# Kernel optimization log

Measured on AMD Instinct MI355X. Metric: run time of the kernel, lower is better.

The kernel has to match this reference:

```python
import jax, jax.numpy as jnp
import numpy as np

MARGIN = 5.0
VAR_FLOOR = 1e-4
BIG = 1e6


def setup_inputs() -> dict:
    key = jax.random.key(0)
    ks = jax.random.split(key, 8)
    B, D, R = 512, 768, 128
    C_new, C_old = 10, 100
    return {
        "features": jax.random.normal(ks[0], (B, D), jnp.float32),
        "labels": jax.random.randint(ks[1], (B,), 0, C_new),
        "new_class_ids": jnp.arange(C_new),
        "cur_means": jax.random.normal(ks[2], (C_new, D), jnp.float32),
        "cur_bases": jax.random.normal(ks[3], (C_new, D, R), jnp.float32),
        "cur_variances": jax.random.uniform(ks[4], (C_new, R + 1), jnp.float32),
        "calibrated_old_means": jax.random.normal(ks[5], (C_old, D), jnp.float32),
        "calibrated_old_bases": jax.random.normal(ks[6], (C_old, D, R), jnp.float32),
        "calibrated_old_variances": jax.random.uniform(ks[7], (C_old, R + 1), jnp.float32),
    }


def _geometry_distance_matrix(z, means, bases, variances):
    # z: [B,D], means: [C,D], bases: [C,D,R], variances: [C,R+1] -> [B,C]
    diff = z[:, None, :] - means[None, :, :]                    # [B,C,D]
    coeff = jnp.einsum('bcd,cdr->bcr', diff, bases)             # [B,C,R]
    eig = jnp.maximum(variances[:, :-1], VAR_FLOOR)             # [C,R]
    res = jnp.maximum(variances[:, -1], VAR_FLOOR)              # [C]
    parallel = jnp.sum(coeff * coeff / eig[None, :, :], axis=-1)  # [B,C]
    recon = jnp.einsum('bcr,cdr->bcd', coeff, bases)            # [B,C,D]
    residual_term = jnp.sum((diff - recon) ** 2, axis=-1) / res[None, :]
    dist = (parallel + residual_term) / z.shape[1]              # normalize_by_dim
    return jnp.nan_to_num(dist, nan=BIG, posinf=BIG, neginf=BIG)


def reference(features, labels, new_class_ids, cur_means, cur_bases, cur_variances,
              calibrated_old_means, calibrated_old_bases, calibrated_old_variances):
    z = jnp.nan_to_num(features, nan=0.0, posinf=0.0, neginf=0.0)  # [B,D]
    labels = labels.reshape(-1)

    own_all = _geometry_distance_matrix(z, cur_means, cur_bases, cur_variances)  # [B,C_new_total]
    old_all = _geometry_distance_matrix(z, calibrated_old_means, calibrated_old_bases,
                                        calibrated_old_variances)               # [B,C_old]
    old_min = jnp.min(old_all, axis=1)                                           # [B]

    # Per-new-class masks; union of class masks reproduces new_mask implicitly.
    masks = (labels[None, :] == new_class_ids[:, None]).astype(z.dtype)          # [K,B]
    counts = masks.sum(axis=1)                                                   # [K]
    denom = jnp.maximum(counts, 1.0)

    own_k = own_all[:, new_class_ids].T                                          # [K,B]
    hinge = jax.nn.relu(MARGIN + own_k - old_min[None, :])                       # [K,B]

    total_k = (hinge * masks).sum(axis=1) / denom
    own_k_mean = (own_k * masks).sum(axis=1) / denom
    old_k_mean = (old_min[None, :] * masks).sum(axis=1) / denom

    valid = (counts > 0).astype(z.dtype)
    n_valid = jnp.maximum(valid.sum(), 1.0)
    total = (total_k * valid).sum() / n_valid
    own = (own_k_mean * valid).sum() / n_valid
    old = (old_k_mean * valid).sum() / n_valid
    return jnp.stack([total, own, old])  # [total, own, old]
```

## Files before the change

### kernel.cpp

```cpp
#include <hip/hip_runtime.h>
#include <hip/hip_bf16.h>
#include <math.h>
#include <stdint.h>

#define B_N   512
#define D_N   768
#define R_N   128
#define C_NEW 10
#define C_OLD 100
#define C_TOT 110
#define MARGIN_F    5.0f
#define VAR_FLOOR_F 1e-4f
#define BIG_F       1e6f

typedef __bf16 bf16;
typedef __bf16 bf16x4 __attribute__((ext_vector_type(4)));
typedef __bf16 bf16x8 __attribute__((ext_vector_type(8)));
typedef float  f32x4  __attribute__((ext_vector_type(4)));

__device__ __forceinline__ float cleanf(float v) { return isfinite(v) ? v : 0.0f; }

__global__ __launch_bounds__(256)
void prep_z(const float* __restrict__ z, bf16* __restrict__ zbf, float* __restrict__ znorm)
{
    const int wave = threadIdx.x >> 6, lane = threadIdx.x & 63;
    const int b = blockIdx.x * 4 + wave;
    const float4* src = (const float4*)(z + (size_t)b * D_N);
    bf16x4* dst = (bf16x4*)(zbf + (size_t)b * D_N);
    float nrm = 0.f;
    #pragma unroll
    for (int i = 0; i < 3; ++i) {
        float4 v = src[lane + i * 64];
        v.x = cleanf(v.x); v.y = cleanf(v.y); v.z = cleanf(v.z); v.w = cleanf(v.w);
        nrm += v.x * v.x + v.y * v.y + v.z * v.z + v.w * v.w;
        bf16x4 w;
        w[0] = (bf16)v.x; w[1] = (bf16)v.y; w[2] = (bf16)v.z; w[3] = (bf16)v.w;
        dst[lane + i * 64] = w;
    }
    #pragma unroll
    for (int off = 32; off >= 1; off >>= 1) nrm += __shfl_xor(nrm, off, 64);
    if (lane == 0) znorm[b] = nrm;
}

__global__ __launch_bounds__(256)
void prep_munorm(const float* __restrict__ cur_means, const float* __restrict__ old_means,
                 float* __restrict__ munorm)
{
    const int c = blockIdx.x;
    const float* mu = (c < C_NEW) ? cur_means + (size_t)c * D_N
                                  : old_means + (size_t)(c - C_NEW) * D_N;
    float p = 0.f;
    for (int d = threadIdx.x; d < D_N; d += 256) p += mu[d] * mu[d];
    #pragma unroll
    for (int off = 32; off >= 1; off >>= 1) p += __shfl_xor(p, off, 64);
    __shared__ float s[4];
    const int wave = threadIdx.x >> 6, lane = threadIdx.x & 63;
    if (lane == 0) s[wave] = p;
    __syncthreads();
    if (threadIdx.x == 0) munorm[c] = s[0] + s[1] + s[2] + s[3];
}

__global__ __launch_bounds__(256)
void transpose_mc(const float* __restrict__ cur_bases, const float* __restrict__ old_bases,
                  const float* __restrict__ cur_means, const float* __restrict__ old_means,
                  bf16* __restrict__ basesT, float* __restrict__ m_c)
{
    const int dt = blockIdx.x, c = blockIdx.y;
    const float* Bc = (c < C_NEW) ? cur_bases + (size_t)c * D_N * R_N
                                  : old_bases + (size_t)(c - C_NEW) * D_N * R_N;
    const float* mu = (c < C_NEW) ? cur_means + (size_t)c * D_N
                                  : old_means + (size_t)(c - C_NEW) * D_N;
    __shared__ bf16 T[128][132];
    __shared__ float sMu[128];
    const int t = threadIdx.x;
    const int d0 = dt * 128;
    if (t < 128) sMu[t] = mu[d0 + t];

    #pragma unroll 4
    for (int it = 0; it < 16; ++it) {
        int q = it * 256 + t;
        int d = q >> 5, rr = (q & 31) * 4;
        float4 v = *(const float4*)(Bc + (size_t)(d0 + d) * R_N + rr);
        T[rr + 0][d] = (bf16)v.x;
        T[rr + 1][d] = (bf16)v.y;
        T[rr + 2][d] = (bf16)v.z;
        T[rr + 3][d] = (bf16)v.w;
    }
    __syncthreads();

    #pragma unroll 4
    for (int it = 0; it < 16; ++it) {
        int q = it * 256 + t;
        int r = q >> 5, dd = (q & 31) * 4;
        ushort4 w = *(const ushort4*)&T[r][dd];
        *(ushort4*)(basesT + (size_t)c * R_N * D_N + (size_t)r * D_N + d0 + dd) = w;
    }

    {
        int r = t & 127, dh = t >> 7;
        float p = 0.f;
        #pragma unroll 8
        for (int k = 0; k < 64; ++k) {
            int d = dh * 64 + k;
            p += sMu[d] * (float)T[r][d];
        }
        atomicAdd(&m_c[c * R_N + r], p);
    }
}

__global__ __launch_bounds__(256)
void gram(const bf16* __restrict__ basesT, bf16* __restrict__ G)
{
    const int c = blockIdx.x;
    const bf16* Tc = basesT + (size_t)c * R_N * D_N;
    __shared__ bf16 sT[128][72];
    const int tid = threadIdx.x, wave = tid >> 6, lane = tid & 63;
    const int quad = lane >> 4, l15 = lane & 15;
    const int wr = (wave >> 1) * 64, wc = (wave & 1) * 64;

    f32x4 acc[4][4];
    #pragma unroll
    for (int i = 0; i < 4; ++i)
        #pragma unroll
        for (int j = 0; j < 4; ++j) acc[i][j] = (f32x4)0.0f;

    for (int k0 = 0; k0 < D_N; k0 += 64) {
        __syncthreads();
        #pragma unroll
        for (int p = 0; p < 4; ++p) {
            int q = p * 256 + tid, row = q >> 3, u = q & 7;
            *(uint4*)(&sT[row][u * 8]) = *(const uint4*)(Tc + (size_t)row * D_N + k0 + u * 8);
        }
        __syncthreads();
        #pragma unroll
        for (int kk = 0; kk < 64; kk += 32) {
            bf16x8 af[4], bg[4];
            #pragma unroll
            for (int i = 0; i < 4; ++i) af[i] = *(const bf16x8*)(&sT[wr + 16 * i + l15][kk + quad * 8]);
            #pragma unroll
            for (int j = 0; j < 4; ++j) bg[j] = *(const bf16x8*)(&sT[wc + 16 * j + l15][kk + quad * 8]);
            #pragma unroll
            for (int i = 0; i < 4; ++i)
                #pragma unroll
                for (int j = 0; j < 4; ++j)
                    acc[i][j] = __builtin_amdgcn_mfma_f32_16x16x32_bf16(af[i], bg[j], acc[i][j], 0, 0, 0);
        }
    }
    #pragma unroll
    for (int i = 0; i < 4; ++i)
        #pragma unroll
        for (int j = 0; j < 4; ++j)
            #pragma unroll
            for (int reg = 0; reg < 4; ++reg) {
                int r = wr + 16 * i + quad * 4 + reg;
                int s = wc + 16 * j + l15;
                G[(size_t)c * 16384 + (size_t)r * 128 + s] = (bf16)acc[i][j][reg];
            }
}

#define PADC 136
#define SM_A   0
#define SM_B   18432
#define SM_G   0
#define SM_C   36864
#define SM_M   (36864 + 34816)
#define SM_INV (SM_M + 512)
#define SM_PAR (SM_INV + 512)
#define SM_CN  (SM_PAR + 512)
#define SM_Q   (SM_CN + 512)
#define SM_T2  (SM_Q + 512)
#define SM_MU  (SM_T2 + 3072)
#define SM_SZ  (SM_MU + 1536)

__global__ __launch_bounds__(256, 2)
void main_dist(const bf16* __restrict__ zbf, const bf16* __restrict__ basesT,
               const bf16* __restrict__ G, const float* __restrict__ m_c,
               const float* __restrict__ cur_vars, const float* __restrict__ old_vars,
               const float* __restrict__ cur_means, const float* __restrict__ old_means,
               const float* __restrict__ znorm, const float* __restrict__ munorm,
               float* __restrict__ gdist)
{
    const int mt = blockIdx.x, c = blockIdx.y;
    const int b0 = mt * 128;
    const float* vars = (c < C_NEW) ? cur_vars + (size_t)c * (R_N + 1)
                                    : old_vars + (size_t)(c - C_NEW) * (R_N + 1);
    const float* mu = (c < C_NEW) ? cur_means + (size_t)c * D_N
                                  : old_means + (size_t)(c - C_NEW) * D_N;
    __shared__ __align__(16) unsigned char smem[SM_SZ];
    bf16*  sA   = (bf16*)(smem + SM_A);
    bf16*  sB   = (bf16*)(smem + SM_B);
    bf16*  sG   = (bf16*)(smem + SM_G);
    bf16*  sC   = (bf16*)(smem + SM_C);
    float* sM   = (float*)(smem + SM_M);
    float* sInv = (float*)(smem + SM_INV);
    float* sPar = (float*)(smem + SM_PAR);
    float* sCn  = (float*)(smem + SM_CN);
    float* sQ   = (float*)(smem + SM_Q);
    float* sT2  = (float*)(smem + SM_T2);
    bf16*  sMuB = (bf16*)(smem + SM_MU);

    const int tid = threadIdx.x, wave = tid >> 6, lane = tid & 63;
    const int quad = lane >> 4, l15 = lane & 15;
    const int wr = (wave >> 1) * 64, wc = (wave & 1) * 64;

    if (tid < 128) {
        sM[tid]   = m_c[c * R_N + tid];
        sInv[tid] = 1.0f / fmaxf(vars[tid], VAR_FLOOR_F);
        sQ[tid]   = 0.0f;
    }
    for (int i = tid; i < D_N; i += 256) sMuB[i] = (bf16)mu[i];

    f32x4 acc1[4][4];
    #pragma unroll
    for (int i = 0; i < 4; ++i)
        #pragma unroll
        for (int j = 0; j < 4; ++j) acc1[i][j] = (f32x4)0.0f;
    float zd = 0.f;
    const int zrow = tid >> 1, zhalf = tid & 1;

    const bf16* Az = zbf + (size_t)b0 * D_N;
    const bf16* Bb = basesT + (size_t)c * R_N * D_N;
    for (int k0 = 0; k0 < D_N; k0 += 64) {
        __syncthreads();
        #pragma unroll
        for (int p = 0; p < 4; ++p) {
            int q = p * 256 + tid, row = q >> 3, u = q & 7;
            *(uint4*)(sA + row * 72 + u * 8) = *(const uint4*)(Az + (size_t)row * D_N + k0 + u * 8);
            *(uint4*)(sB + row * 72 + u * 8) = *(const uint4*)(Bb + (size_t)row * D_N + k0 + u * 8);
        }
        __syncthreads();
        #pragma unroll
        for (int kk = 0; kk < 64; kk += 32) {
            bf16x8 af[4], bg[4];
            #pragma unroll
            for (int i = 0; i < 4; ++i) af[i] = *(const bf16x8*)(sA + (wr + 16 * i + l15) * 72 + kk + quad * 8);
            #pragma unroll
            for (int j = 0; j < 4; ++j) bg[j] = *(const bf16x8*)(sB + (wc + 16 * j + l15) * 72 + kk + quad * 8);
            #pragma unroll
            for (int i = 0; i < 4; ++i)
                #pragma unroll
                for (int j = 0; j < 4; ++j)
                    acc1[i][j] = __builtin_amdgcn_mfma_f32_16x16x32_bf16(af[i], bg[j], acc1[i][j], 0, 0, 0);
        }
        {
            const bf16* zr = sA + zrow * 72 + zhalf * 32;
            const bf16* mr = sMuB + k0 + zhalf * 32;
            #pragma unroll
            for (int m = 0; m < 4; ++m) {
                bf16x8 a = *(const bf16x8*)(zr + m * 8);
                bf16x8 b = *(const bf16x8*)(mr + m * 8);
                #pragma unroll
                for (int e = 0; e < 8; ++e) zd += (float)a[e] * (float)b[e];
            }
        }
    }
    sT2[512 + tid] = zd;

    #pragma unroll
    for (int j = 0; j < 4; ++j) {
        float mcv = sM[wc + 16 * j + l15];
        #pragma unroll
        for (int i = 0; i < 4; ++i)
            #pragma unroll
            for (int reg = 0; reg < 4; ++reg) {
                float cv = acc1[i][j][reg] - mcv;
                acc1[i][j][reg] = cv;
                int row = wr + 16 * i + quad * 4 + reg;
                int col = wc + 16 * j + l15;
                sC[row * PADC + col] = (bf16)cv;
            }
    }
    __syncthreads();

    {
        int row = tid >> 1, half = tid & 1;
        float par = 0.f, cn = 0.f;
        #pragma unroll
        for (int m = 0; m < 8; ++m) {
            bf16x8 v = *(const bf16x8*)(sC + row * PADC + half * 64 + m * 8);
            #pragma unroll
            for (int e = 0; e < 8; ++e) {
                float f = (float)v[e];
                int col = half * 64 + m * 8 + e;
                cn  += f * f;
                par += f * f * sInv[col];
            }
        }
        sT2[tid] = par;
        sT2[256 + tid] = cn;
    }
    #pragma unroll
    for (int p = 0; p < 8; ++p) {
        int q = p * 256 + tid, s = q >> 4, u = q & 15;
        *(uint4*)(sG + s * PADC + u * 8) = *(const uint4*)(G + (size_t)c * 16384 + (size_t)s * 128 + u * 8);
    }
    __syncthreads();
    if (tid < 128) {
        sPar[tid] = sT2[tid * 2] + sT2[tid * 2 + 1];
        sCn[tid]  = sT2[256 + tid * 2] + sT2[256 + tid * 2 + 1];
    }

    f32x4 acc2[4][4];
    #pragma unroll
    for (int i = 0; i < 4; ++i)
        #pragma unroll
        for (int j = 0; j < 4; ++j) acc2[i][j] = (f32x4)0.0f;
    #pragma unroll
    for (int kc = 0; kc < 128; kc += 32) {
        bf16x8 af[4], bg[4];
        #pragma unroll
        for (int i = 0; i < 4; ++i) af[i] = *(const bf16x8*)(sC + (wr + 16 * i + l15) * PADC + kc + quad * 8);
        #pragma unroll
        for (int j = 0; j < 4; ++j) bg[j] = *(const bf16x8*)(sG + (wc + 16 * j + l15) * PADC + kc + quad * 8);
        #pragma unroll
        for (int i = 0; i < 4; ++i)
            #pragma unroll
            for (int j = 0; j < 4; ++j)
                acc2[i][j] = __builtin_amdgcn_mfma_f32_16x16x32_bf16(af[i], bg[j], acc2[i][j], 0, 0, 0);
    }

    #pragma unroll
    for (int i = 0; i < 4; ++i)
        #pragma unroll
        for (int reg = 0; reg < 4; ++reg) {
            float qp = 0.f;
            #pragma unroll
            for (int j = 0; j < 4; ++j) qp += acc2[i][j][reg] * acc1[i][j][reg];
            qp += __shfl_xor(qp, 1, 64);
            qp += __shfl_xor(qp, 2, 64);
            qp += __shfl_xor(qp, 4, 64);
            qp += __shfl_xor(qp, 8, 64);
            if (l15 == 0) atomicAdd(&sQ[wr + 16 * i + quad * 4 + reg], qp);
        }
    __syncthreads();

    if (tid < 128) {
        int b = b0 + tid;
        float zdot = sT2[512 + tid * 2] + sT2[512 + tid * 2 + 1];
        float nd2 = znorm[b] - 2.0f * zdot + munorm[c];
        float res = fmaxf(vars[R_N], VAR_FLOOR_F);
        float dist = (sPar[tid] + (nd2 - 2.0f * sCn[tid] + sQ[tid]) / res) / (float)D_N;
        if (!isfinite(dist)) dist = BIG_F;
        gdist[(size_t)b * C_TOT + c] = dist;
    }
}

__global__ __launch_bounds__(64)
void finalize_stage1(const float* __restrict__ gdist,
                     const int* __restrict__ labels,
                     const int* __restrict__ ncid,
                     float* __restrict__ acc)
{
    const int b = blockIdx.x * 64 + threadIdx.x;
    const float* row = gdist + (size_t)b * C_TOT;
    float mn = 3.4e38f;
    #pragma unroll
    for (int cc = C_NEW; cc < C_TOT; ++cc) mn = fminf(mn, row[cc]);
    const int lab = labels[b];
    #pragma unroll
    for (int k = 0; k < C_NEW; ++k) {
        if (lab == ncid[k]) {
            int col = min(max(ncid[k], 0), C_TOT - 1);
            float ow = row[col];
            atomicAdd(&acc[k * 4 + 0], 1.0f);
            atomicAdd(&acc[k * 4 + 1], fmaxf(0.0f, MARGIN_F + ow - mn));
            atomicAdd(&acc[k * 4 + 2], ow);
            atomicAdd(&acc[k * 4 + 3], mn);
        }
    }
}

__global__ __launch_bounds__(64)
void finalize_stage2(const float* __restrict__ acc, float* __restrict__ out)
{
    if (threadIdx.x == 0) {
        float total = 0.f, own = 0.f, old = 0.f, nv = 0.f;
        #pragma unroll
        for (int k = 0; k < C_NEW; ++k) {
            float cnt = acc[k * 4 + 0];
            float den = fmaxf(cnt, 1.0f);
            if (cnt > 0.f) {
                nv += 1.f;
                total += acc[k * 4 + 1] / den;
                own   += acc[k * 4 + 2] / den;
                old   += acc[k * 4 + 3] / den;
            }
        }
        float nvd = fmaxf(nv, 1.0f);
        out[0] = total / nvd;
        out[1] = own / nvd;
        out[2] = old / nvd;
    }
}

extern "C" void kernel_launch(void* const* d_in, const int* in_sizes, int n_in,
                              void* d_out, int out_size, void* d_ws, size_t ws_size,
                              hipStream_t stream)
{
    const float* features  = (const float*)d_in[0];
    const int*   labels    = (const int*)d_in[1];
    const int*   ncid      = (const int*)d_in[2];
    const float* cur_means = (const float*)d_in[3];
    const float* cur_bases = (const float*)d_in[4];
    const float* cur_vars  = (const float*)d_in[5];
    const float* old_means = (const float*)d_in[6];
    const float* old_bases = (const float*)d_in[7];
    const float* old_vars  = (const float*)d_in[8];

    unsigned char* ws = (unsigned char*)d_ws;
    float* gdist  = (float*)(ws + 0);
    bf16*  zbf    = (bf16*) (ws + 225280);
    float* znorm  = (float*)(ws + 1011712);
    float* munorm = (float*)(ws + 1013760);
    float* m_c    = (float*)(ws + 1014272);
    float* acc    = (float*)(ws + 1070592);
    bf16*  basesT = (bf16*) (ws + 1070848);
    bf16*  G      = (bf16*) (ws + 22697728);

    hipMemsetAsync(m_c, 0, 56320 + 256, stream);

    prep_z<<<dim3(128), dim3(256), 0, stream>>>(features, zbf, znorm);
    prep_munorm<<<dim3(C_TOT), dim3(256), 0, stream>>>(cur_means, old_means, munorm);
    transpose_mc<<<dim3(6, C_TOT), dim3(256), 0, stream>>>(cur_bases, old_bases,
                                                           cur_means, old_means,
                                                           basesT, m_c);
    gram<<<dim3(C_TOT), dim3(256), 0, stream>>>(basesT, G);
    main_dist<<<dim3(4, C_TOT), dim3(256), 0, stream>>>(zbf, basesT, G, m_c,
                                                        cur_vars, old_vars,
                                                        cur_means, old_means,
                                                        znorm, munorm, gdist);
    finalize_stage1<<<dim3(8), dim3(64), 0, stream>>>(gdist, labels, ncid, acc);
    finalize_stage2<<<dim3(1), dim3(64), 0, stream>>>(acc, (float*)d_out);
}
```

Measured before the change: 163.8 us.

## Fuse basis transpose, Gram, and mean projections into one per-class kernel

Merges prep_munorm, transpose_mc and gram into a single per-class prep_bases kernel. It transposes each 128-row chunk of the basis into LDS, feeds the Gram MFMA straight from that tile, and computes m_c without atomics, which removes the basesT re-read and the memset of m_c. main_dist now stages its A, B and G tiles with global_load_lds direct-to-LDS loads into unpadded layouts. The fused kernel runs only 110 blocks, so the transpose has less parallelism. The unpadded LDS strides may also cause bank conflicts in the MFMA operand reads.

```diff
diff --git a/kernel.cpp b/kernel.cpp
--- a/kernel.cpp
+++ b/kernel.cpp
@@ -20,6 +20,12 @@
 
 __device__ __forceinline__ float cleanf(float v) { return isfinite(v) ? v : 0.0f; }
 
+__device__ __forceinline__ void gld16(const bf16* g, bf16* l) {
+    __builtin_amdgcn_global_load_lds(
+        (const __attribute__((address_space(1))) unsigned int*)g,
+        (__attribute__((address_space(3))) unsigned int*)l, 16, 0, 0);
+}
+
 __global__ __launch_bounds__(256)
 void prep_z(const float* __restrict__ z, bf16* __restrict__ zbf, float* __restrict__ znorm)
 {
@@ -43,80 +49,35 @@
 }
 
 __global__ __launch_bounds__(256)
-void prep_munorm(const float* __restrict__ cur_means, const float* __restrict__ old_means,
-                 float* __restrict__ munorm)
+void prep_bases(const float* __restrict__ cur_bases, const float* __restrict__ old_bases,
+                const float* __restrict__ cur_means, const float* __restrict__ old_means,
+                bf16* __restrict__ basesT, bf16* __restrict__ G,
+                float* __restrict__ m_c, float* __restrict__ munorm)
 {
     const int c = blockIdx.x;
-    const float* mu = (c < C_NEW) ? cur_means + (size_t)c * D_N
-                                  : old_means + (size_t)(c - C_NEW) * D_N;
-    float p = 0.f;
-    for (int d = threadIdx.x; d < D_N; d += 256) p += mu[d] * mu[d];
-    #pragma unroll
-    for (int off = 32; off >= 1; off >>= 1) p += __shfl_xor(p, off, 64);
-    __shared__ float s[4];
-    const int wave = threadIdx.x >> 6, lane = threadIdx.x & 63;
-    if (lane == 0) s[wave] = p;
-    __syncthreads();
-    if (threadIdx.x == 0) munorm[c] = s[0] + s[1] + s[2] + s[3];
-}
-
-__global__ __launch_bounds__(256)
-void transpose_mc(const float* __restrict__ cur_bases, const float* __restrict__ old_bases,
-                  const float* __restrict__ cur_means, const float* __restrict__ old_means,
-                  bf16* __restrict__ basesT, float* __restrict__ m_c)
-{
-    const int dt = blockIdx.x, c = blockIdx.y;
     const float* Bc = (c < C_NEW) ? cur_bases + (size_t)c * D_N * R_N
                                   : old_bases + (size_t)(c - C_NEW) * D_N * R_N;
     const float* mu = (c < C_NEW) ? cur_means + (size_t)c * D_N
                                   : old_means + (size_t)(c - C_NEW) * D_N;
-    __shared__ bf16 T[128][132];
-    __shared__ float sMu[128];
-    const int t = threadIdx.x;
-    const int d0 = dt * 128;
-    if (t < 128) sMu[t] = mu[d0 + t];
-
-    #pragma unroll 4
-    for (int it = 0; it < 16; ++it) {
-        int q = it * 256 + t;
-        int d = q >> 5, rr = (q & 31) * 4;
-        float4 v = *(const float4*)(Bc + (size_t)(d0 + d) * R_N + rr);
-        T[rr + 0][d] = (bf16)v.x;
-        T[rr + 1][d] = (bf16)v.y;
-        T[rr + 2][d] = (bf16)v.z;
-        T[rr + 3][d] = (bf16)v.w;
-    }
-    __syncthreads();
-
-    #pragma unroll 4
-    for (int it = 0; it < 16; ++it) {
-        int q = it * 256 + t;
-        int r = q >> 5, dd = (q & 31) * 4;
-        ushort4 w = *(const ushort4*)&T[r][dd];
-        *(ushort4*)(basesT + (size_t)c * R_N * D_N + (size_t)r * D_N + d0 + dd) = w;
-    }
-
-    {
-        int r = t & 127, dh = t >> 7;
-        float p = 0.f;
-        #pragma unroll 8
-        for (int k = 0; k < 64; ++k) {
-            int d = dh * 64 + k;
-            p += sMu[d] * (float)T[r][d];
-        }
-        atomicAdd(&m_c[c * R_N + r], p);
-    }
-}
-
-__global__ __launch_bounds__(256)
-void gram(const bf16* __restrict__ basesT, bf16* __restrict__ G)
-{
-    const int c = blockIdx.x;
-    const bf16* Tc = basesT + (size_t)c * R_N * D_N;
-    __shared__ bf16 sT[128][72];
+
+    __shared__ bf16 T[128][136];
+    __shared__ float sMu[D_N];
+    __shared__ float sRed[256];
+
     const int tid = threadIdx.x, wave = tid >> 6, lane = tid & 63;
     const int quad = lane >> 4, l15 = lane & 15;
-    const int wr = (wave >> 1) * 64, wc = (wave & 1) * 64;
+    const int wr = (wave >> 1) * 64, wcn = (wave & 1) * 64;
+
+    float mn = 0.f;
+    for (int i = tid; i < D_N; i += 256) { float v = mu[i]; sMu[i] = v; mn += v * v; }
+    #pragma unroll
+    for (int off = 32; off >= 1; off >>= 1) mn += __shfl_xor(mn, off, 64);
+    if (lane == 0) sRed[wave] = mn;
+    __syncthreads();
+    if (tid == 0) munorm[c] = sRed[0] + sRed[1] + sRed[2] + sRed[3];
+
+    float mcAcc = 0.f;
+    const int mr = tid & 127, mdh = tid >> 7;
 
     f32x4 acc[4][4];
     #pragma unroll
@@ -124,21 +85,47 @@
         #pragma unroll
         for (int j = 0; j < 4; ++j) acc[i][j] = (f32x4)0.0f;
 
-    for (int k0 = 0; k0 < D_N; k0 += 64) {
+    for (int ch = 0; ch < 6; ++ch) {
+        const int d0 = ch * 128;
         __syncthreads();
         #pragma unroll
-        for (int p = 0; p < 4; ++p) {
-            int q = p * 256 + tid, row = q >> 3, u = q & 7;
-            *(uint4*)(&sT[row][u * 8]) = *(const uint4*)(Tc + (size_t)row * D_N + k0 + u * 8);
+        for (int m = 0; m < 2; ++m) {
+            int u = m * 256 + tid;
+            int r4 = (u & 31) * 4;
+            int dg = u >> 5;
+            float4 v[8];
+            #pragma unroll
+            for (int j = 0; j < 8; ++j)
+                v[j] = *(const float4*)(Bc + (size_t)(d0 + dg * 8 + j) * R_N + r4);
+            #pragma unroll
+            for (int i = 0; i < 4; ++i) {
+                bf16x8 w;
+                #pragma unroll
+                for (int j = 0; j < 8; ++j) {
+                    float f = (i == 0) ? v[j].x : (i == 1) ? v[j].y : (i == 2) ? v[j].z : v[j].w;
+                    w[j] = (bf16)f;
+                }
+                *(bf16x8*)&T[r4 + i][dg * 8] = w;
+            }
         }
         __syncthreads();
-        #pragma unroll
-        for (int kk = 0; kk < 64; kk += 32) {
+        {
+            int r = tid >> 1, hf = tid & 1;
+            const uint4* srcp = (const uint4*)&T[r][hf * 64];
+            uint4* dstp = (uint4*)(basesT + (size_t)c * R_N * D_N + (size_t)r * D_N + d0 + hf * 64);
+            #pragma unroll
+            for (int m2 = 0; m2 < 8; ++m2) dstp[m2] = srcp[m2];
+        }
+        #pragma unroll 8
+        for (int k = 0; k < 64; ++k)
+            mcAcc += sMu[d0 + mdh * 64 + k] * (float)T[mr][mdh * 64 + k];
+        #pragma unroll
+        for (int kk = 0; kk < 128; kk += 32) {
             bf16x8 af[4], bg[4];
             #pragma unroll
-            for (int i = 0; i < 4; ++i) af[i] = *(const bf16x8*)(&sT[wr + 16 * i + l15][kk + quad * 8]);
-            #pragma unroll
-            for (int j = 0; j < 4; ++j) bg[j] = *(const bf16x8*)(&sT[wc + 16 * j + l15][kk + quad * 8]);
+            for (int i = 0; i < 4; ++i) af[i] = *(const bf16x8*)&T[wr + 16 * i + l15][kk + quad * 8];
+            #pragma unroll
+            for (int j = 0; j < 4; ++j) bg[j] = *(const bf16x8*)&T[wcn + 16 * j + l15][kk + quad * 8];
             #pragma unroll
             for (int i = 0; i < 4; ++i)
                 #pragma unroll
@@ -146,6 +133,11 @@
                     acc[i][j] = __builtin_amdgcn_mfma_f32_16x16x32_bf16(af[i], bg[j], acc[i][j], 0, 0, 0);
         }
     }
+    __syncthreads();
+    sRed[tid] = mcAcc;
+    __syncthreads();
+    if (tid < 128) m_c[c * R_N + tid] = sRed[tid] + sRed[128 + tid];
+
     #pragma unroll
     for (int i = 0; i < 4; ++i)
         #pragma unroll
@@ -153,24 +145,22 @@
             #pragma unroll
             for (int reg = 0; reg < 4; ++reg) {
                 int r = wr + 16 * i + quad * 4 + reg;
-                int s = wc + 16 * j + l15;
+                int s = wcn + 16 * j + l15;
                 G[(size_t)c * 16384 + (size_t)r * 128 + s] = (bf16)acc[i][j][reg];
             }
 }
 
 #define PADC 136
-#define SM_A   0
-#define SM_B   18432
-#define SM_G   0
-#define SM_C   36864
-#define SM_M   (36864 + 34816)
-#define SM_INV (SM_M + 512)
-#define SM_PAR (SM_INV + 512)
-#define SM_CN  (SM_PAR + 512)
-#define SM_Q   (SM_CN + 512)
-#define SM_T2  (SM_Q + 512)
-#define SM_MU  (SM_T2 + 3072)
-#define SM_SZ  (SM_MU + 1536)
+#define SM_AB  0
+#define SM_C   32768
+#define SM_M   67584
+#define SM_INV 68096
+#define SM_PAR 68608
+#define SM_CN  69120
+#define SM_Q   69632
+#define SM_T2  70144
+#define SM_MU  73216
+#define SM_SZ  74752
 
 __global__ __launch_bounds__(256, 2)
 void main_dist(const bf16* __restrict__ zbf, const bf16* __restrict__ basesT,
@@ -187,9 +177,9 @@
     const float* mu = (c < C_NEW) ? cur_means + (size_t)c * D_N
                                   : old_means + (size_t)(c - C_NEW) * D_N;
     __shared__ __align__(16) unsigned char smem[SM_SZ];
-    bf16*  sA   = (bf16*)(smem + SM_A);
-    bf16*  sB   = (bf16*)(smem + SM_B);
-    bf16*  sG   = (bf16*)(smem + SM_G);
+    bf16*  sA   = (bf16*)(smem + SM_AB);
+    bf16*  sB   = (bf16*)(smem + SM_AB + 16384);
+    bf16*  sG   = (bf16*)(smem + SM_AB);
     bf16*  sC   = (bf16*)(smem + SM_C);
     float* sM   = (float*)(smem + SM_M);
     float* sInv = (float*)(smem + SM_INV);
@@ -220,22 +210,25 @@
 
     const bf16* Az = zbf + (size_t)b0 * D_N;
     const bf16* Bb = basesT + (size_t)c * R_N * D_N;
+    const int rl = lane >> 3;
+    const int cl = lane & 7;
+
     for (int k0 = 0; k0 < D_N; k0 += 64) {
         __syncthreads();
         #pragma unroll
-        for (int p = 0; p < 4; ++p) {
-            int q = p * 256 + tid, row = q >> 3, u = q & 7;
-            *(uint4*)(sA + row * 72 + u * 8) = *(const uint4*)(Az + (size_t)row * D_N + k0 + u * 8);
-            *(uint4*)(sB + row * 72 + u * 8) = *(const uint4*)(Bb + (size_t)row * D_N + k0 + u * 8);
+        for (int j = 0; j < 4; ++j) {
+            int r0 = j * 32 + wave * 8;
+            gld16(Az + (size_t)(r0 + rl) * D_N + k0 + cl * 8, sA + r0 * 64);
+            gld16(Bb + (size_t)(r0 + rl) * D_N + k0 + cl * 8, sB + r0 * 64);
         }
         __syncthreads();
         #pragma unroll
         for (int kk = 0; kk < 64; kk += 32) {
             bf16x8 af[4], bg[4];
             #pragma unroll
-            for (int i = 0; i < 4; ++i) af[i] = *(const bf16x8*)(sA + (wr + 16 * i + l15) * 72 + kk + quad * 8);
-            #pragma unroll
-            for (int j = 0; j < 4; ++j) bg[j] = *(const bf16x8*)(sB + (wc + 16 * j + l15) * 72 + kk + quad * 8);
+            for (int i = 0; i < 4; ++i) af[i] = *(const bf16x8*)(sA + (wr + 16 * i + l15) * 64 + kk + quad * 8);
+            #pragma unroll
+            for (int j = 0; j < 4; ++j) bg[j] = *(const bf16x8*)(sB + (wc + 16 * j + l15) * 64 + kk + quad * 8);
             #pragma unroll
             for (int i = 0; i < 4; ++i)
                 #pragma unroll
@@ -243,7 +236,7 @@
                     acc1[i][j] = __builtin_amdgcn_mfma_f32_16x16x32_bf16(af[i], bg[j], acc1[i][j], 0, 0, 0);
         }
         {
-            const bf16* zr = sA + zrow * 72 + zhalf * 32;
+            const bf16* zr = sA + zrow * 64 + zhalf * 32;
             const bf16* mr = sMuB + k0 + zhalf * 32;
             #pragma unroll
             for (int m = 0; m < 4; ++m) {
@@ -289,10 +282,13 @@
         sT2[tid] = par;
         sT2[256 + tid] = cn;
     }
-    #pragma unroll
-    for (int p = 0; p < 8; ++p) {
-        int q = p * 256 + tid, s = q >> 4, u = q & 15;
-        *(uint4*)(sG + s * PADC + u * 8) = *(const uint4*)(G + (size_t)c * 16384 + (size_t)s * 128 + u * 8);
+    {
+        const bf16* Gc = G + (size_t)c * 16384;
+        #pragma unroll
+        for (int j = 0; j < 8; ++j) {
+            int off = (wave * 8 + j) * 512;
+            gld16(Gc + off + lane * 8, sG + off);
+        }
     }
     __syncthreads();
     if (tid < 128) {
@@ -311,7 +307,7 @@
         #pragma unroll
         for (int i = 0; i < 4; ++i) af[i] = *(const bf16x8*)(sC + (wr + 16 * i + l15) * PADC + kc + quad * 8);
         #pragma unroll
-        for (int j = 0; j < 4; ++j) bg[j] = *(const bf16x8*)(sG + (wc + 16 * j + l15) * PADC + kc + quad * 8);
+        for (int j = 0; j < 4; ++j) bg[j] = *(const bf16x8*)(sG + (wc + 16 * j + l15) * 128 + kc + quad * 8);
         #pragma unroll
         for (int i = 0; i < 4; ++i)
             #pragma unroll
@@ -417,14 +413,12 @@
     bf16*  basesT = (bf16*) (ws + 1070848);
     bf16*  G      = (bf16*) (ws + 22697728);
 
-    hipMemsetAsync(m_c, 0, 56320 + 256, stream);
+    hipMemsetAsync(acc, 0, 256, stream);
 
     prep_z<<<dim3(128), dim3(256), 0, stream>>>(features, zbf, znorm);
-    prep_munorm<<<dim3(C_TOT), dim3(256), 0, stream>>>(cur_means, old_means, munorm);
-    transpose_mc<<<dim3(6, C_TOT), dim3(256), 0, stream>>>(cur_bases, old_bases,
-                                                           cur_means, old_means,
-                                                           basesT, m_c);
-    gram<<<dim3(C_TOT), dim3(256), 0, stream>>>(basesT, G);
+    prep_bases<<<dim3(C_TOT), dim3(256), 0, stream>>>(cur_bases, old_bases,
+                                                      cur_means, old_means,
+                                                      basesT, G, m_c, munorm);
     main_dist<<<dim3(4, C_TOT), dim3(256), 0, stream>>>(zbf, basesT, G, m_c,
                                                         cur_vars, old_vars,
                                                         cur_means, old_means,
```

After: 170.1 us. 3.8% more time.
